# Kernel optimization log

Measured on AMD Instinct MI355X. Metric: run time of the kernel, lower is better.

Reference implementation:

```python
import jax, jax.numpy as jnp
import numpy as np

N_NODES = 100000
N_EDGES = 1600000
D_IN = 128
D_HID = 64
N_CLASSES = 64


def setup_inputs() -> dict:
    key = jax.random.key(0)
    ks = jax.random.split(key, 12)
    x = jax.random.normal(ks[0], (N_NODES, D_IN), dtype=jnp.float32)
    edge_index = jax.random.randint(ks[1], (2, N_EDGES), 0, N_NODES, dtype=jnp.int64)
    def lin(k, fan_in, fan_out):
        k1, k2 = jax.random.split(k)
        bound = 1.0 / np.sqrt(fan_in)
        w = jax.random.uniform(k1, (fan_in, fan_out), jnp.float32, -bound, bound)
        b = jax.random.uniform(k2, (fan_out,), jnp.float32, -bound, bound)
        return w, b
    w1a, b1a = lin(ks[2], D_IN, D_HID)
    w1b, b1b = lin(ks[3], D_HID, D_HID)
    w2a, b2a = lin(ks[4], D_HID, D_HID)
    w2b, b2b = lin(ks[5], D_HID, N_CLASSES)
    return {"x": x, "edge_index": edge_index,
            "w1a": w1a, "b1a": b1a, "w1b": w1b, "b1b": b1b,
            "w2a": w2a, "b2a": b2a, "w2b": w2b, "b2b": b2b}


def _gin_agg(x, src, dst):
    # GINConv with eps=0: (1+eps)*x_i + sum_{j->i} x_j
    agg = jax.ops.segment_sum(x[src], dst, num_segments=N_NODES)
    return x + agg


def reference(x, edge_index, w1a, b1a, w1b, b1b, w2a, b2a, w2b, b2b):
    src, dst = edge_index[0], edge_index[1]
    # conv1: MLP = Linear -> ReLU -> Linear -> ReLU
    h = _gin_agg(x, src, dst)
    h = jax.nn.relu(h @ w1a + b1a)
    h = jax.nn.relu(h @ w1b + b1b)
    # conv2: MLP = Linear -> ReLU -> Linear
    h = _gin_agg(h, src, dst)
    h = jax.nn.relu(h @ w2a + b2a)
    h = h @ w2b + b2b
    # global add pool over the single graph -> [1, num_classes]
    return jnp.sum(h, axis=0, keepdims=True)
```

## Files before the change

### kernel.cpp

```cpp
#include <hip/hip_runtime.h>

#define N_NODES 100000
#define N_EDGES 1600000
#define D_IN 128
#define D 64

#define NBLK 1000
#define EPB  1600
#define NB2  391
#define SC_M  (NB2 * NBLK)
#define SC_CH 1024
#define SC_NB ((SC_M + SC_CH - 1) / SC_CH)

__device__ __forceinline__ float bf2f(unsigned short u) {
    union { unsigned int i; float f; } q; q.i = ((unsigned int)u) << 16; return q.f;
}
__device__ __forceinline__ unsigned short f2bf(float f) {
    unsigned int u = __float_as_uint(f);
    unsigned int r = (u + 0x7FFFu + ((u >> 16) & 1u)) >> 16;
    return (unsigned short)r;
}
__device__ __forceinline__ void acc4(float4& a, ushort4 v) {
    a.x += bf2f(v.x); a.y += bf2f(v.y); a.z += bf2f(v.z); a.w += bf2f(v.w);
}


__global__ __launch_bounds__(256) void k_hist1(const int* __restrict__ dst,
                                               int* __restrict__ bh) {
    __shared__ int h[NB2];
    int t = threadIdx.x;
    for (int i = t; i < NB2; i += 256) h[i] = 0;
    __syncthreads();
    int base = blockIdx.x * EPB;
    for (int i = t; i < EPB; i += 256) atomicAdd(&h[dst[base + i] >> 8], 1);
    __syncthreads();
    for (int i = t; i < NB2; i += 256) bh[i * NBLK + blockIdx.x] = h[i];
}

__global__ __launch_bounds__(256) void k_scanA(const int* __restrict__ bh,
                                               int* __restrict__ part) {
    __shared__ int s[256];
    int t = threadIdx.x;
    int base = blockIdx.x * SC_CH + t * 4;
    int sum = 0;
    if (base + 3 < SC_M) {
        int4 v = *(const int4*)(bh + base);
        sum = (v.x + v.y) + (v.z + v.w);
    } else {
        for (int k = 0; k < 4; k++) if (base + k < SC_M) sum += bh[base + k];
    }
    s[t] = sum;
    __syncthreads();
    for (int o = 128; o > 0; o >>= 1) {
        if (t < o) s[t] += s[t + o];
        __syncthreads();
    }
    if (t == 0) part[blockIdx.x] = s[0];
}

__global__ __launch_bounds__(512) void k_scanB(int* __restrict__ part) {
    __shared__ int s[512];
    int t = threadIdx.x;
    int v = (t < SC_NB) ? part[t] : 0;
    s[t] = v;
    __syncthreads();
    for (int o = 1; o < 512; o <<= 1) {
        int x = (t >= o) ? s[t - o] : 0;
        __syncthreads();
        s[t] += x;
        __syncthreads();
    }
    if (t < SC_NB) part[t] = s[t] - v;
}

__global__ __launch_bounds__(256) void k_scanC(int* __restrict__ bh,
                                               const int* __restrict__ part) {
    __shared__ int s[256];
    int t = threadIdx.x;
    int base = blockIdx.x * SC_CH + t * 4;
    int4 v = {0, 0, 0, 0};
    if (base + 3 < SC_M) v = *(const int4*)(bh + base);
    else { for (int k = 0; k < 4; k++) if (base + k < SC_M) (&v.x)[k] = bh[base + k]; }
    int sum = (v.x + v.y) + (v.z + v.w);
    s[t] = sum;
    __syncthreads();
    for (int o = 1; o < 256; o <<= 1) {
        int x = (t >= o) ? s[t - o] : 0;
        __syncthreads();
        s[t] += x;
        __syncthreads();
    }
    int run = part[blockIdx.x] + s[t] - sum;
    int4 w;
    w.x = run; run += v.x;
    w.y = run; run += v.y;
    w.z = run; run += v.z;
    w.w = run;
    if (base + 3 < SC_M) *(int4*)(bh + base) = w;
    else { for (int k = 0; k < 4; k++) if (base + k < SC_M) bh[base + k] = (&w.x)[k]; }
}

__global__ __launch_bounds__(256) void k_scatter1(const int* __restrict__ src,
                                                  const int* __restrict__ dst,
                                                  const int* __restrict__ bh,
                                                  uint2* __restrict__ tmp) {
    __shared__ int cur[NB2];
    int t = threadIdx.x;
    for (int i = t; i < NB2; i += 256) cur[i] = bh[i * NBLK + blockIdx.x];
    __syncthreads();
    int base = blockIdx.x * EPB;
    for (int i = t; i < EPB; i += 256) {
        int d = dst[base + i];
        int sv = src[base + i];
        int p = atomicAdd(&cur[d >> 8], 1);
        tmp[p] = make_uint2((unsigned)d, (unsigned)sv);
    }
}

__global__ __launch_bounds__(256) void k_padsum(const uint2* __restrict__ tmp,
                                                const int* __restrict__ bh,
                                                int* __restrict__ degarr,
                                                int* __restrict__ pb) {
    __shared__ int deg[256];
    __shared__ int s[256];
    int b = blockIdx.x, t = threadIdx.x;
    int e0 = bh[b * NBLK];
    int e1 = (b == NB2 - 1) ? N_EDGES : bh[(b + 1) * NBLK];
    deg[t] = 0;
    __syncthreads();
    for (int i = e0 + t; i < e1; i += 256) atomicAdd(&deg[tmp[i].x & 255u], 1);
    __syncthreads();
    int node = b * 256 + t;
    int d = (node < N_NODES) ? deg[t] : 0;
    if (node < N_NODES) degarr[node] = d;
    int dp = (d + 15) & ~15;
    s[t] = dp;
    __syncthreads();
    for (int o = 128; o > 0; o >>= 1) {
        if (t < o) s[t] += s[t + o];
        __syncthreads();
    }
    if (t == 0) pb[b] = s[0];
}

__global__ __launch_bounds__(512) void k_scanP(int* __restrict__ pb) {
    __shared__ int s[512];
    int t = threadIdx.x;
    int v = (t < NB2) ? pb[t] : 0;
    s[t] = v;
    __syncthreads();
    for (int o = 1; o < 512; o <<= 1) {
        int x = (t >= o) ? s[t - o] : 0;
        __syncthreads();
        s[t] += x;
        __syncthreads();
    }
    if (t < NB2) pb[t] = s[t] - v;
}

__global__ __launch_bounds__(256) void k_build2(const uint2* __restrict__ tmp,
                                                const int* __restrict__ bh,
                                                const int* __restrict__ degarr,
                                                const int* __restrict__ pb,
                                                int* __restrict__ offs,
                                                int* __restrict__ csr) {
    __shared__ int s[256];
    __shared__ int startp[256];
    __shared__ int cur[256];
    int b = blockIdx.x, t = threadIdx.x;
    int e0 = bh[b * NBLK];
    int e1 = (b == NB2 - 1) ? N_EDGES : bh[(b + 1) * NBLK];
    int node = b * 256 + t;
    int d = (node < N_NODES) ? degarr[node] : 0;
    int dp = (d + 15) & ~15;
    s[t] = dp;
    __syncthreads();
    for (int o = 1; o < 256; o <<= 1) {
        int x = (t >= o) ? s[t - o] : 0;
        __syncthreads();
        s[t] += x;
        __syncthreads();
    }
    int st = pb[b] + s[t] - dp;
    startp[t] = st;
    cur[t] = st;
    if (node < N_NODES) {
        offs[node] = st;
        if (node == N_NODES - 1) offs[N_NODES] = st + dp;
    }
    __syncthreads();
    for (int i = e0 + t; i < e1; i += 256) {
        uint2 p = tmp[i];
        int pos = atomicAdd(&cur[p.x & 255u], 1);
        csr[pos] = (int)p.y;
    }
    __syncthreads();
    int end = startp[t] + dp;
    for (int p = cur[t]; p < end; p++) csr[p] = N_NODES;
}

__global__ __launch_bounds__(256) void k_gemm1(const float* __restrict__ x,
                                               const float* __restrict__ w,
                                               unsigned short* __restrict__ z) {
    __shared__ float ws[D_IN][D];
    __shared__ float xs[16][D_IN + 1];
    int t = threadIdx.x;
    {
        const float4* w4 = (const float4*)w;
        float4* s4 = (float4*)&ws[0][0];
        for (int i = t; i < (D_IN * D) / 4; i += 256) s4[i] = w4[i];
    }
    int r = t >> 4, c = t & 15;
    __syncthreads();
    for (int base = blockIdx.x * 16; base < N_NODES; base += gridDim.x * 16) {
        for (int i = t; i < 16 * (D_IN / 4); i += 256) {
            int row = i >> 5, k4 = i & 31;
            float4 v = ((const float4*)(x + (size_t)(base + row) * D_IN))[k4];
            xs[row][k4 * 4 + 0] = v.x; xs[row][k4 * 4 + 1] = v.y;
            xs[row][k4 * 4 + 2] = v.z; xs[row][k4 * 4 + 3] = v.w;
        }
        __syncthreads();
        float4 acc = {0.f, 0.f, 0.f, 0.f};
        for (int k = 0; k < D_IN; k++) {
            float xv = xs[r][k];
            float4 wv = *(const float4*)&ws[k][c * 4];
            acc.x += xv * wv.x; acc.y += xv * wv.y;
            acc.z += xv * wv.z; acc.w += xv * wv.w;
        }
        ushort4 p;
        p.x = f2bf(acc.x); p.y = f2bf(acc.y); p.z = f2bf(acc.z); p.w = f2bf(acc.w);
        *(ushort4*)(z + (size_t)(base + r) * D + c * 4) = p;
        __syncthreads();
    }
}

__device__ __forceinline__ void gather16p(float4& acc, const unsigned short* __restrict__ zz,
                                          const int* __restrict__ csr,
                                          int e0, int e1, size_t c4) {
    for (int e = e0; e < e1; e += 16) {
        int idx[16];
        *(int4*)(&idx[0])  = *(const int4*)(csr + e);
        *(int4*)(&idx[4])  = *(const int4*)(csr + e + 4);
        *(int4*)(&idx[8])  = *(const int4*)(csr + e + 8);
        *(int4*)(&idx[12]) = *(const int4*)(csr + e + 12);
        ushort4 vv[16];
        #pragma unroll
        for (int k = 0; k < 16; k++)
            vv[k] = *(const ushort4*)(zz + (size_t)idx[k] * D + c4);
        #pragma unroll
        for (int k = 0; k < 16; k++) acc4(acc, vv[k]);
    }
}

__global__ __launch_bounds__(256, 6) void k_conv1(const unsigned short* __restrict__ z,
                                                  const int* __restrict__ offs,
                                                  const int* __restrict__ csr,
                                                  const float* __restrict__ b1a,
                                                  const float* __restrict__ w1b,
                                                  const float* __restrict__ b1b,
                                                  const float* __restrict__ w2a,
                                                  unsigned short* __restrict__ u) {
    __shared__ unsigned short w1s[D][D];
    __shared__ unsigned short w2s[D][D];
    __shared__ float h1s[16][D + 1];
    __shared__ float h2s[16][D + 1];
    int t = threadIdx.x;
    int r = t >> 4, c = t & 15;
    {
        for (int i = t; i < (D * D) / 4; i += 256) {
            float4 a = ((const float4*)w1b)[i];
            ushort4 p; p.x = f2bf(a.x); p.y = f2bf(a.y); p.z = f2bf(a.z); p.w = f2bf(a.w);
            *(ushort4*)&(&w1s[0][0])[i * 4] = p;
            float4 b = ((const float4*)w2a)[i];
            ushort4 q; q.x = f2bf(b.x); q.y = f2bf(b.y); q.z = f2bf(b.z); q.w = f2bf(b.w);
            *(ushort4*)&(&w2s[0][0])[i * 4] = q;
        }
    }
    float4 vb1a = ((const float4*)b1a)[c];
    float4 vb1b = ((const float4*)b1b)[c];
    __syncthreads();

    const size_t c4 = (size_t)(c * 4);
    for (int base = blockIdx.x * 16; base < N_NODES; base += gridDim.x * 16) {
        int node = base + r;
        float4 acc = {vb1a.x, vb1a.y, vb1a.z, vb1a.w};
        acc4(acc, *(const ushort4*)(z + (size_t)node * D + c4));
        int e0 = offs[node], e1 = offs[node + 1];
        gather16p(acc, z, csr, e0, e1, c4);
        h1s[r][c * 4 + 0] = fmaxf(acc.x, 0.f);
        h1s[r][c * 4 + 1] = fmaxf(acc.y, 0.f);
        h1s[r][c * 4 + 2] = fmaxf(acc.z, 0.f);
        h1s[r][c * 4 + 3] = fmaxf(acc.w, 0.f);
        __syncthreads();
        float4 a2 = vb1b;
        for (int k = 0; k < D; k++) {
            float hv = h1s[r][k];
            ushort4 wv = *(const ushort4*)&w1s[k][c * 4];
            a2.x += hv * bf2f(wv.x); a2.y += hv * bf2f(wv.y);
            a2.z += hv * bf2f(wv.z); a2.w += hv * bf2f(wv.w);
        }
        h2s[r][c * 4 + 0] = fmaxf(a2.x, 0.f);
        h2s[r][c * 4 + 1] = fmaxf(a2.y, 0.f);
        h2s[r][c * 4 + 2] = fmaxf(a2.z, 0.f);
        h2s[r][c * 4 + 3] = fmaxf(a2.w, 0.f);
        __syncthreads();
        float4 a3 = {0.f, 0.f, 0.f, 0.f};
        for (int k = 0; k < D; k++) {
            float hv = h2s[r][k];
            ushort4 wv = *(const ushort4*)&w2s[k][c * 4];
            a3.x += hv * bf2f(wv.x); a3.y += hv * bf2f(wv.y);
            a3.z += hv * bf2f(wv.z); a3.w += hv * bf2f(wv.w);
        }
        ushort4 p;
        p.x = f2bf(a3.x); p.y = f2bf(a3.y); p.z = f2bf(a3.z); p.w = f2bf(a3.w);
        *(ushort4*)(u + (size_t)node * D + c4) = p;
        __syncthreads();
    }
}

__global__ __launch_bounds__(256) void k_conv2(const unsigned short* __restrict__ u,
                                               const int* __restrict__ offs,
                                               const int* __restrict__ csr,
                                               const float* __restrict__ b2a,
                                               float* __restrict__ colsum) {
    __shared__ float red[16][D + 1];
    int t = threadIdx.x;
    int r = t >> 4, c = t & 15;
    float4 vb = ((const float4*)b2a)[c];
    float4 cs = {0.f, 0.f, 0.f, 0.f};
    const size_t c4 = (size_t)(c * 4);
    for (int base = blockIdx.x * 16; base < N_NODES; base += gridDim.x * 16) {
        int node = base + r;
        float4 acc = {vb.x, vb.y, vb.z, vb.w};
        acc4(acc, *(const ushort4*)(u + (size_t)node * D + c4));
        int e0 = offs[node], e1 = offs[node + 1];
        gather16p(acc, u, csr, e0, e1, c4);
        cs.x += fmaxf(acc.x, 0.f); cs.y += fmaxf(acc.y, 0.f);
        cs.z += fmaxf(acc.z, 0.f); cs.w += fmaxf(acc.w, 0.f);
    }
    red[r][c * 4 + 0] = cs.x; red[r][c * 4 + 1] = cs.y;
    red[r][c * 4 + 2] = cs.z; red[r][c * 4 + 3] = cs.w;
    __syncthreads();
    if (r == 0) {
        float4 tot = {0.f, 0.f, 0.f, 0.f};
        for (int rr = 0; rr < 16; rr++) {
            tot.x += red[rr][c * 4 + 0]; tot.y += red[rr][c * 4 + 1];
            tot.z += red[rr][c * 4 + 2]; tot.w += red[rr][c * 4 + 3];
        }
        atomicAdd(&colsum[c * 4 + 0], tot.x);
        atomicAdd(&colsum[c * 4 + 1], tot.y);
        atomicAdd(&colsum[c * 4 + 2], tot.z);
        atomicAdd(&colsum[c * 4 + 3], tot.w);
    }
}

__global__ void k_final(const float* __restrict__ colsum, const float* __restrict__ w2b,
                        const float* __restrict__ b2b, float* __restrict__ out) {
    int j = threadIdx.x;
    float acc = (float)N_NODES * b2b[j];
    for (int k = 0; k < D; k++) acc += colsum[k] * w2b[k * D + j];
    out[j] = acc;
}


extern "C" void kernel_launch(void* const* d_in, const int* in_sizes, int n_in,
                              void* d_out, int out_size, void* d_ws, size_t ws_size,
                              hipStream_t stream) {
    const float* x   = (const float*)d_in[0];
    const int*   ei  = (const int*)d_in[1];
    const float* w1a = (const float*)d_in[2];
    const float* b1a = (const float*)d_in[3];
    const float* w1b = (const float*)d_in[4];
    const float* b1b = (const float*)d_in[5];
    const float* w2a = (const float*)d_in[6];
    const float* b2a = (const float*)d_in[7];
    const float* w2b = (const float*)d_in[8];
    const float* b2b = (const float*)d_in[9];
    float* out = (float*)d_out;

    const int* srcp = ei;
    const int* dstp = ei + N_EDGES;

    char* ws = (char*)d_ws;
    unsigned short* z = (unsigned short*)(ws + 0);
    unsigned short* u = (unsigned short*)(ws + 12800256);
    uint2* tmp    = (uint2*)(ws + 25600512);
    int*   csr    = (int*)(ws + 38400512);
    int*   bh     = (int*)(ws + 51200512);
    int*   degarr = (int*)(ws + 52764512);
    int*   offs   = (int*)(ws + 53164896);
    int*   pb     = (int*)(ws + 53564960);
    int*   part   = (int*)(ws + 53567008);
    float* colsum = (float*)(ws + 53569056);

    hipMemsetAsync(colsum, 0, D * sizeof(float), stream);
    hipMemsetAsync(z + (size_t)N_NODES * D, 0, D * sizeof(unsigned short), stream);
    hipMemsetAsync(u + (size_t)N_NODES * D, 0, D * sizeof(unsigned short), stream);

    k_hist1   <<<NBLK, 256, 0, stream>>>(dstp, bh);
    k_scanA   <<<SC_NB, 256, 0, stream>>>(bh, part);
    k_scanB   <<<1, 512, 0, stream>>>(part);
    k_scanC   <<<SC_NB, 256, 0, stream>>>(bh, part);
    k_scatter1<<<NBLK, 256, 0, stream>>>(srcp, dstp, bh, tmp);
    k_padsum  <<<NB2, 256, 0, stream>>>(tmp, bh, degarr, pb);
    k_scanP   <<<1, 512, 0, stream>>>(pb);
    k_build2  <<<NB2, 256, 0, stream>>>(tmp, bh, degarr, pb, offs, csr);

    k_gemm1<<<2048, 256, 0, stream>>>(x, w1a, z);
    k_conv1<<<2048, 256, 0, stream>>>(z, offs, csr, b1a, w1b, b1b, w2a, u);
    k_conv2<<<2048, 256, 0, stream>>>(u, offs, csr, b2a, colsum);
    k_final<<<1, 64, 0, stream>>>(colsum, w2b, b2b, out);
}
```

Measured before the change: 485.3 us.

## Widen gather loads to 16 bytes per thread and pad CSR to 8

```diff
diff --git a/kernel.cpp b/kernel.cpp
--- a/kernel.cpp
+++ b/kernel.cpp
@@ -12,16 +12,22 @@
 #define SC_CH 1024
 #define SC_NB ((SC_M + SC_CH - 1) / SC_CH)
 
-__device__ __forceinline__ float bf2f(unsigned short u) {
-    union { unsigned int i; float f; } q; q.i = ((unsigned int)u) << 16; return q.f;
+__device__ __forceinline__ float bflo(unsigned int u) {
+    union { unsigned int i; float f; } q; q.i = u << 16; return q.f;
+}
+__device__ __forceinline__ float bfhi(unsigned int u) {
+    union { unsigned int i; float f; } q; q.i = u & 0xFFFF0000u; return q.f;
 }
 __device__ __forceinline__ unsigned short f2bf(float f) {
     unsigned int u = __float_as_uint(f);
     unsigned int r = (u + 0x7FFFu + ((u >> 16) & 1u)) >> 16;
     return (unsigned short)r;
 }
-__device__ __forceinline__ void acc4(float4& a, ushort4 v) {
-    a.x += bf2f(v.x); a.y += bf2f(v.y); a.z += bf2f(v.z); a.w += bf2f(v.w);
+__device__ __forceinline__ void accU4(float* a, uint4 v) {
+    a[0] += bflo(v.x); a[1] += bfhi(v.x);
+    a[2] += bflo(v.y); a[3] += bfhi(v.y);
+    a[4] += bflo(v.z); a[5] += bfhi(v.z);
+    a[6] += bflo(v.w); a[7] += bfhi(v.w);
 }
 
 
@@ -133,7 +139,7 @@
     int node = b * 256 + t;
     int d = (node < N_NODES) ? deg[t] : 0;
     if (node < N_NODES) degarr[node] = d;
-    int dp = (d + 15) & ~15;
+    int dp = (d + 7) & ~7;
     s[t] = dp;
     __syncthreads();
     for (int o = 128; o > 0; o >>= 1) {
@@ -172,7 +178,7 @@
     int e1 = (b == NB2 - 1) ? N_EDGES : bh[(b + 1) * NBLK];
     int node = b * 256 + t;
     int d = (node < N_NODES) ? degarr[node] : 0;
-    int dp = (d + 15) & ~15;
+    int dp = (d + 7) & ~7;
     s[t] = dp;
     __syncthreads();
     for (int o = 1; o < 256; o <<= 1) {
@@ -234,25 +240,25 @@
     }
 }
 
-__device__ __forceinline__ void gather16p(float4& acc, const unsigned short* __restrict__ zz,
-                                          const int* __restrict__ csr,
-                                          int e0, int e1, size_t c4) {
-    for (int e = e0; e < e1; e += 16) {
-        int idx[16];
-        *(int4*)(&idx[0])  = *(const int4*)(csr + e);
-        *(int4*)(&idx[4])  = *(const int4*)(csr + e + 4);
-        *(int4*)(&idx[8])  = *(const int4*)(csr + e + 8);
-        *(int4*)(&idx[12]) = *(const int4*)(csr + e + 12);
-        ushort4 vv[16];
-        #pragma unroll
-        for (int k = 0; k < 16; k++)
-            vv[k] = *(const ushort4*)(zz + (size_t)idx[k] * D + c4);
-        #pragma unroll
-        for (int k = 0; k < 16; k++) acc4(acc, vv[k]);
-    }
-}
-
-__global__ __launch_bounds__(256, 6) void k_conv1(const unsigned short* __restrict__ z,
+__device__ __forceinline__ void gather8p(float* acc, const unsigned short* __restrict__ zz,
+                                         const int* __restrict__ csr,
+                                         int e0, int e1, int c) {
+    const char* zb = (const char*)zz;
+    for (int e = e0; e < e1; e += 8) {
+        int idx[8];
+        *(int4*)(&idx[0]) = *(const int4*)(csr + e);
+        *(int4*)(&idx[4]) = *(const int4*)(csr + e + 4);
+        uint4 vv[8];
+        #pragma unroll
+        for (int k = 0; k < 8; k++)
+            vv[k] = *(const uint4*)(zb + (size_t)idx[k] * 128 + c * 16);
+        #pragma unroll
+        for (int k = 0; k < 8; k++) accU4(acc, vv[k]);
+    }
+}
+
+#define HS 68
+__global__ __launch_bounds__(256, 4) void k_conv1(const unsigned short* __restrict__ z,
                                                   const int* __restrict__ offs,
                                                   const int* __restrict__ csr,
                                                   const float* __restrict__ b1a,
@@ -262,10 +268,10 @@
                                                   unsigned short* __restrict__ u) {
     __shared__ unsigned short w1s[D][D];
     __shared__ unsigned short w2s[D][D];
-    __shared__ float h1s[16][D + 1];
-    __shared__ float h2s[16][D + 1];
-    int t = threadIdx.x;
-    int r = t >> 4, c = t & 15;
+    __shared__ float h1s[32][HS];
+    __shared__ float h2s[32][HS];
+    int t = threadIdx.x;
+    int r = t >> 3, c = t & 7;
     {
         for (int i = t; i < (D * D) / 4; i += 256) {
             float4 a = ((const float4*)w1b)[i];
@@ -276,81 +282,104 @@
             *(ushort4*)&(&w2s[0][0])[i * 4] = q;
         }
     }
-    float4 vb1a = ((const float4*)b1a)[c];
-    float4 vb1b = ((const float4*)b1b)[c];
-    __syncthreads();
-
-    const size_t c4 = (size_t)(c * 4);
-    for (int base = blockIdx.x * 16; base < N_NODES; base += gridDim.x * 16) {
+    float vb1a[8], vb1b[8];
+    {
+        float4 a0 = ((const float4*)b1a)[c * 2], a1 = ((const float4*)b1a)[c * 2 + 1];
+        vb1a[0] = a0.x; vb1a[1] = a0.y; vb1a[2] = a0.z; vb1a[3] = a0.w;
+        vb1a[4] = a1.x; vb1a[5] = a1.y; vb1a[6] = a1.z; vb1a[7] = a1.w;
+        float4 b0 = ((const float4*)b1b)[c * 2], b1 = ((const float4*)b1b)[c * 2 + 1];
+        vb1b[0] = b0.x; vb1b[1] = b0.y; vb1b[2] = b0.z; vb1b[3] = b0.w;
+        vb1b[4] = b1.x; vb1b[5] = b1.y; vb1b[6] = b1.z; vb1b[7] = b1.w;
+    }
+    __syncthreads();
+
+    for (int base = blockIdx.x * 32; base < N_NODES; base += gridDim.x * 32) {
         int node = base + r;
-        float4 acc = {vb1a.x, vb1a.y, vb1a.z, vb1a.w};
-        acc4(acc, *(const ushort4*)(z + (size_t)node * D + c4));
+        float acc[8];
+        #pragma unroll
+        for (int j = 0; j < 8; j++) acc[j] = vb1a[j];
+        accU4(acc, *(const uint4*)((const char*)z + (size_t)node * 128 + c * 16));
         int e0 = offs[node], e1 = offs[node + 1];
-        gather16p(acc, z, csr, e0, e1, c4);
-        h1s[r][c * 4 + 0] = fmaxf(acc.x, 0.f);
-        h1s[r][c * 4 + 1] = fmaxf(acc.y, 0.f);
-        h1s[r][c * 4 + 2] = fmaxf(acc.z, 0.f);
-        h1s[r][c * 4 + 3] = fmaxf(acc.w, 0.f);
-        __syncthreads();
-        float4 a2 = vb1b;
+        gather8p(acc, z, csr, e0, e1, c);
+        *(float4*)&h1s[r][c * 8]     = make_float4(fmaxf(acc[0], 0.f), fmaxf(acc[1], 0.f),
+                                                   fmaxf(acc[2], 0.f), fmaxf(acc[3], 0.f));
+        *(float4*)&h1s[r][c * 8 + 4] = make_float4(fmaxf(acc[4], 0.f), fmaxf(acc[5], 0.f),
+                                                   fmaxf(acc[6], 0.f), fmaxf(acc[7], 0.f));
+        __syncthreads();
+        float a2[8];
+        #pragma unroll
+        for (int j = 0; j < 8; j++) a2[j] = vb1b[j];
         for (int k = 0; k < D; k++) {
             float hv = h1s[r][k];
-            ushort4 wv = *(const ushort4*)&w1s[k][c * 4];
-            a2.x += hv * bf2f(wv.x); a2.y += hv * bf2f(wv.y);
-            a2.z += hv * bf2f(wv.z); a2.w += hv * bf2f(wv.w);
-        }
-        h2s[r][c * 4 + 0] = fmaxf(a2.x, 0.f);
-        h2s[r][c * 4 + 1] = fmaxf(a2.y, 0.f);
-        h2s[r][c * 4 + 2] = fmaxf(a2.z, 0.f);
-        h2s[r][c * 4 + 3] = fmaxf(a2.w, 0.f);
-        __syncthreads();
-        float4 a3 = {0.f, 0.f, 0.f, 0.f};
+            uint4 w = *(const uint4*)&w1s[k][c * 8];
+            a2[0] += hv * bflo(w.x); a2[1] += hv * bfhi(w.x);
+            a2[2] += hv * bflo(w.y); a2[3] += hv * bfhi(w.y);
+            a2[4] += hv * bflo(w.z); a2[5] += hv * bfhi(w.z);
+            a2[6] += hv * bflo(w.w); a2[7] += hv * bfhi(w.w);
+        }
+        *(float4*)&h2s[r][c * 8]     = make_float4(fmaxf(a2[0], 0.f), fmaxf(a2[1], 0.f),
+                                                   fmaxf(a2[2], 0.f), fmaxf(a2[3], 0.f));
+        *(float4*)&h2s[r][c * 8 + 4] = make_float4(fmaxf(a2[4], 0.f), fmaxf(a2[5], 0.f),
+                                                   fmaxf(a2[6], 0.f), fmaxf(a2[7], 0.f));
+        __syncthreads();
+        float a3[8] = {0.f, 0.f, 0.f, 0.f, 0.f, 0.f, 0.f, 0.f};
         for (int k = 0; k < D; k++) {
             float hv = h2s[r][k];
-            ushort4 wv = *(const ushort4*)&w2s[k][c * 4];
-            a3.x += hv * bf2f(wv.x); a3.y += hv * bf2f(wv.y);
-            a3.z += hv * bf2f(wv.z); a3.w += hv * bf2f(wv.w);
-        }
-        ushort4 p;
-        p.x = f2bf(a3.x); p.y = f2bf(a3.y); p.z = f2bf(a3.z); p.w = f2bf(a3.w);
-        *(ushort4*)(u + (size_t)node * D + c4) = p;
-        __syncthreads();
-    }
-}
-
-__global__ __launch_bounds__(256) void k_conv2(const unsigned short* __restrict__ u,
-                                               const int* __restrict__ offs,
-                                               const int* __restrict__ csr,
-                                               const float* __restrict__ b2a,
-                                               float* __restrict__ colsum) {
-    __shared__ float red[16][D + 1];
-    int t = threadIdx.x;
-    int r = t >> 4, c = t & 15;
-    float4 vb = ((const float4*)b2a)[c];
-    float4 cs = {0.f, 0.f, 0.f, 0.f};
-    const size_t c4 = (size_t)(c * 4);
-    for (int base = blockIdx.x * 16; base < N_NODES; base += gridDim.x * 16) {
+            uint4 w = *(const uint4*)&w2s[k][c * 8];
+            a3[0] += hv * bflo(w.x); a3[1] += hv * bfhi(w.x);
+            a3[2] += hv * bflo(w.y); a3[3] += hv * bfhi(w.y);
+            a3[4] += hv * bflo(w.z); a3[5] += hv * bfhi(w.z);
+            a3[6] += hv * bflo(w.w); a3[7] += hv * bfhi(w.w);
+        }
+        uint4 p;
+        p.x = ((unsigned)f2bf(a3[1]) << 16) | f2bf(a3[0]);
+        p.y = ((unsigned)f2bf(a3[3]) << 16) | f2bf(a3[2]);
+        p.z = ((unsigned)f2bf(a3[5]) << 16) | f2bf(a3[4]);
+        p.w = ((unsigned)f2bf(a3[7]) << 16) | f2bf(a3[6]);
+        *(uint4*)((char*)u + (size_t)node * 128 + c * 16) = p;
+        __syncthreads();
+    }
+}
+
+__global__ __launch_bounds__(256, 6) void k_conv2(const unsigned short* __restrict__ u,
+                                                  const int* __restrict__ offs,
+                                                  const int* __restrict__ csr,
+                                                  const float* __restrict__ b2a,
+                                                  float* __restrict__ colsum) {
+    __shared__ float red[32][HS];
+    int t = threadIdx.x;
+    int r = t >> 3, c = t & 7;
+    float vb[8];
+    {
+        float4 a0 = ((const float4*)b2a)[c * 2], a1 = ((const float4*)b2a)[c * 2 + 1];
+        vb[0] = a0.x; vb[1] = a0.y; vb[2] = a0.z; vb[3] = a0.w;
+        vb[4] = a1.x; vb[5] = a1.y; vb[6] = a1.z; vb[7] = a1.w;
+    }
+    float cs[8] = {0.f, 0.f, 0.f, 0.f, 0.f, 0.f, 0.f, 0.f};
+    for (int base = blockIdx.x * 32; base < N_NODES; base += gridDim.x * 32) {
         int node = base + r;
-        float4 acc = {vb.x, vb.y, vb.z, vb.w};
-        acc4(acc, *(const ushort4*)(u + (size_t)node * D + c4));
+        float acc[8];
+        #pragma unroll
+        for (int j = 0; j < 8; j++) acc[j] = vb[j];
+        accU4(acc, *(const uint4*)((const char*)u + (size_t)node * 128 + c * 16));
         int e0 = offs[node], e1 = offs[node + 1];
-        gather16p(acc, u, csr, e0, e1, c4);
-        cs.x += fmaxf(acc.x, 0.f); cs.y += fmaxf(acc.y, 0.f);
-        cs.z += fmaxf(acc.z, 0.f); cs.w += fmaxf(acc.w, 0.f);
-    }
-    red[r][c * 4 + 0] = cs.x; red[r][c * 4 + 1] = cs.y;
-    red[r][c * 4 + 2] = cs.z; red[r][c * 4 + 3] = cs.w;
-    __syncthreads();
-    if (r == 0) {
-        float4 tot = {0.f, 0.f, 0.f, 0.f};
-        for (int rr = 0; rr < 16; rr++) {
-            tot.x += red[rr][c * 4 + 0]; tot.y += red[rr][c * 4 + 1];
-            tot.z += red[rr][c * 4 + 2]; tot.w += red[rr][c * 4 + 3];
-        }
-        atomicAdd(&colsum[c * 4 + 0], tot.x);
-        atomicAdd(&colsum[c * 4 + 1], tot.y);
-        atomicAdd(&colsum[c * 4 + 2], tot.z);
-        atomicAdd(&colsum[c * 4 + 3], tot.w);
+        gather8p(acc, u, csr, e0, e1, c);
+        #pragma unroll
+        for (int j = 0; j < 8; j++) cs[j] += fmaxf(acc[j], 0.f);
+    }
+    *(float4*)&red[r][c * 8]     = make_float4(cs[0], cs[1], cs[2], cs[3]);
+    *(float4*)&red[r][c * 8 + 4] = make_float4(cs[4], cs[5], cs[6], cs[7]);
+    for (int off = 16; off >= 1; off >>= 1) {
+        __syncthreads();
+        if (r < off) {
+            #pragma unroll
+            for (int j = 0; j < 8; j++) red[r][c * 8 + j] += red[r + off][c * 8 + j];
+        }
+    }
+    __syncthreads();
+    if (t < 8) {
+        #pragma unroll
+        for (int j = 0; j < 8; j++) atomicAdd(&colsum[t * 8 + j], red[0][t * 8 + j]);
     }
 }
 
```

Result: slower. 686.3 us (+41.4%).
